# Kernel tuning notes

Measured on AMD Instinct MI355X. Metric: run time of the kernel, lower is better.

The kernel has to match this reference:

```python
import jax, jax.numpy as jnp
import numpy as np

R_EARTH = 6371.0


def haversine(coords):
    # coords: (B, N, 2) lat/lon in degrees -> (B, N, N) distances in km
    lat = jnp.deg2rad(coords[..., 0])
    lon = jnp.deg2rad(coords[..., 1])
    lat1, lon1 = lat[:, :, None], lon[:, :, None]   # (B,N,1)
    lat2, lon2 = lat[:, None, :], lon[:, None, :]   # (B,1,N)
    dlat, dlon = lat2 - lat1, lon2 - lon1
    a = jnp.sin(dlat / 2) ** 2 + jnp.cos(lat1) * jnp.cos(lat2) * jnp.sin(dlon / 2) ** 2
    a = jnp.clip(a, 0.0, 1.0)
    c = 2.0 * jnp.arctan2(jnp.sqrt(a), jnp.sqrt(1.0 - a))
    return R_EARTH * c


def setup_inputs() -> dict:
    key = jax.random.key(0)
    ks = jax.random.split(key, 16)
    B, N, T, D, H = 4, 256, 128, 512, 8
    hd = D // H
    s = 1.0 / np.sqrt(D)
    inp = {
        'x': jax.random.normal(ks[0], (B, N, T, D), dtype=jnp.float32),
        'coords': jax.random.uniform(ks[1], (B, N, 2), dtype=jnp.float32) * 90.0,
        'station_mask': jax.random.randint(ks[2], (B, N), 0, 2, dtype=jnp.int32),
        'Wq': jax.random.normal(ks[3], (D, D), dtype=jnp.float32) * s,
        'bq': jnp.zeros((D,), dtype=jnp.float32),
        'Wk': jax.random.normal(ks[4], (D, D), dtype=jnp.float32) * s,
        'bk': jnp.zeros((D,), dtype=jnp.float32),
        'Wv': jax.random.normal(ks[5], (D, D), dtype=jnp.float32) * s,
        'bv': jnp.zeros((D,), dtype=jnp.float32),
        'Wo': jax.random.normal(ks[6], (D, D), dtype=jnp.float32) * s,
        'bo': jnp.zeros((D,), dtype=jnp.float32),
        'Wd1': jax.random.normal(ks[7], (hd, 1), dtype=jnp.float32),
        'bd1': jnp.zeros((hd,), dtype=jnp.float32),
        'Wd2': jax.random.normal(ks[8], (H, hd), dtype=jnp.float32) / np.sqrt(hd),
        'bd2': jnp.zeros((H,), dtype=jnp.float32),
    }
    return inp


def reference(x, coords, station_mask, Wq, bq, Wk, bk, Wv, bv, Wo, bo, Wd1, bd1, Wd2, bd2):
    B, N, T, D = x.shape
    H = Wd2.shape[0]
    hd = D // H
    scale = jnp.sqrt(jnp.asarray(hd, dtype=x.dtype))

    x_repr = x.mean(axis=2)  # (B,N,D) temporal pooling

    def proj(W, b):
        y = x_repr @ W.T + b                       # (B,N,D)
        return y.reshape(B, N, H, hd).transpose(0, 2, 1, 3)  # (B,H,N,hd)

    Q, K, V = proj(Wq, bq), proj(Wk, bk), proj(Wv, bv)
    scores = jnp.einsum('bhnd,bhmd->bhnm', Q, K) / scale  # (B,H,N,N)

    # haversine distance -> 2-layer MLP bias, (B,N,N,H) -> (B,H,N,N)
    dist = haversine(coords)[..., None]                    # (B,N,N,1)
    hmid = jax.nn.relu(dist @ Wd1.T + bd1)                 # (B,N,N,hd)
    bias = (hmid @ Wd2.T + bd2).transpose(0, 3, 1, 2)      # (B,H,N,N)
    scores = scores + bias

    # mask invalid key stations
    scores = jnp.where(station_mask[:, None, None, :] == 0, -jnp.inf, scores)
    w = jax.nn.softmax(scores, axis=-1)

    out = jnp.einsum('bhnm,bhmd->bhnd', w, V)
    out = out.transpose(0, 2, 1, 3).reshape(B, N, D)
    out = out @ Wo.T + bo
    return jnp.broadcast_to(out[:, :, None, :], (B, N, T, D))
```

## Files before the change

kernel.cpp:

```cpp
#include <hip/hip_runtime.h>
#include <math.h>

#define Bc 4
#define Nc 256
#define Tc 128
#define Dc 512
#define Hc 8
#define HDc 64

__device__ __forceinline__ float4 f4add(float4 a, float4 b) {
    return make_float4(a.x + b.x, a.y + b.y, a.z + b.z, a.w + b.w);
}

#define SWZ(row, k4) (((row) << 4) | ((k4) ^ (((row) >> 2) & 15)))

__global__ __launch_bounds__(256) void mean_kernel(const float* __restrict__ x,
                                                   float* __restrict__ xr) {
    const int bn = blockIdx.x;
    const int col = threadIdx.x & 127;
    const int half = threadIdx.x >> 7;
    const float4* xp = (const float4*)x + (size_t)bn * (Tc * Dc / 4)
                       + (size_t)(half * 64) * (Dc / 4) + col;
    float4 a0 = make_float4(0.f, 0.f, 0.f, 0.f), a1 = a0, a2 = a0, a3 = a0;
    for (int t = 0; t < 64; t += 4) {
        a0 = f4add(a0, xp[(size_t)(t + 0) * (Dc / 4)]);
        a1 = f4add(a1, xp[(size_t)(t + 1) * (Dc / 4)]);
        a2 = f4add(a2, xp[(size_t)(t + 2) * (Dc / 4)]);
        a3 = f4add(a3, xp[(size_t)(t + 3) * (Dc / 4)]);
    }
    __shared__ float4 red[256];
    red[threadIdx.x] = f4add(f4add(a0, a1), f4add(a2, a3));
    __syncthreads();
    if (threadIdx.x < 128) {
        float4 s = f4add(red[threadIdx.x], red[threadIdx.x + 128]);
        const float r = 1.0f / Tc;
        ((float4*)xr)[(size_t)bn * (Dc / 4) + threadIdx.x] =
            make_float4(s.x * r, s.y * r, s.z * r, s.w * r);
    }
}

__device__ __forceinline__ void gemm_core(const float* __restrict__ A,
                                          const float* __restrict__ W,
                                          int i0, int j0, float acc[4][4]) {
    __shared__ float4 As4[1024];
    __shared__ float4 Ws4[1024];
    const int tid = threadIdx.x;
    const int ty = tid >> 4, tx = tid & 15;
    for (int kb = 0; kb < 8; ++kb) {
        const int k0 = kb * 64;
#pragma unroll
        for (int p = 0; p < 4; ++p) {
            const int idx = p * 256 + tid;
            const int row = idx >> 4, k4 = idx & 15;
            As4[SWZ(row, k4)] = *(const float4*)&A[(size_t)(i0 + row) * Dc + k0 + k4 * 4];
            Ws4[SWZ(row, k4)] = *(const float4*)&W[(size_t)(j0 + row) * Dc + k0 + k4 * 4];
        }
        __syncthreads();
#pragma unroll
        for (int kk4 = 0; kk4 < 16; ++kk4) {
            float4 a[4], w[4];
#pragma unroll
            for (int q = 0; q < 4; ++q) a[q] = As4[SWZ(ty * 4 + q, kk4)];
#pragma unroll
            for (int c = 0; c < 4; ++c) w[c] = Ws4[SWZ(tx * 4 + c, kk4)];
#pragma unroll
            for (int q = 0; q < 4; ++q)
#pragma unroll
                for (int c = 0; c < 4; ++c) {
                    acc[q][c] += a[q].x * w[c].x;
                    acc[q][c] += a[q].y * w[c].y;
                    acc[q][c] += a[q].z * w[c].z;
                    acc[q][c] += a[q].w * w[c].w;
                }
        }
        __syncthreads();
    }
}

__global__ __launch_bounds__(256) void qkv_kernel(
    const float* __restrict__ xr, const float* __restrict__ Wq, const float* __restrict__ bq,
    const float* __restrict__ Wk, const float* __restrict__ bk,
    const float* __restrict__ Wv, const float* __restrict__ bv,
    float* __restrict__ Yq, float* __restrict__ Kt, float* __restrict__ Yv) {
    const int it = blockIdx.x;
    const int mat = blockIdx.y >> 3;
    const int jt = blockIdx.y & 7;
    const float* W = (mat == 0) ? Wq : (mat == 1) ? Wk : Wv;
    const float* bias = (mat == 0) ? bq : (mat == 1) ? bk : bv;
    const int i0 = it * 64, j0 = jt * 64;
    float acc[4][4] = {{0.f}};
    gemm_core(xr, W, i0, j0, acc);
    const int ty = threadIdx.x >> 4, tx = threadIdx.x & 15;
    if (mat == 1) {
        const int b = i0 >> 8;
        const int n0 = (i0 & 255) + ty * 4;
#pragma unroll
        for (int c = 0; c < 4; ++c) {
            const int j = j0 + tx * 4 + c;
            const float bj = bias[j];
            float4 v = make_float4(acc[0][c] + bj, acc[1][c] + bj,
                                   acc[2][c] + bj, acc[3][c] + bj);
            *(float4*)&Kt[(((size_t)b * Hc + jt) * HDc + (tx * 4 + c)) * Nc + n0] = v;
        }
    } else {
        float* Y = (mat == 0) ? Yq : Yv;
#pragma unroll
        for (int r = 0; r < 4; ++r) {
            const int i = i0 + ty * 4 + r;
            const int j = j0 + tx * 4;
            float4 o = make_float4(acc[r][0] + bias[j + 0], acc[r][1] + bias[j + 1],
                                   acc[r][2] + bias[j + 2], acc[r][3] + bias[j + 3]);
            *(float4*)&Y[(size_t)i * Dc + j] = o;
        }
    }
}

__global__ __launch_bounds__(256) void oproj_kernel(const float* __restrict__ attn,
                                                    const float* __restrict__ Wo,
                                                    const float* __restrict__ bo,
                                                    float* __restrict__ Y) {
    const int i0 = blockIdx.x * 64, j0 = blockIdx.y * 64;
    float acc[4][4] = {{0.f}};
    gemm_core(attn, Wo, i0, j0, acc);
    const int ty = threadIdx.x >> 4, tx = threadIdx.x & 15;
#pragma unroll
    for (int r = 0; r < 4; ++r) {
        const int i = i0 + ty * 4 + r;
        const int j = j0 + tx * 4;
        float4 o = make_float4(acc[r][0] + bo[j + 0], acc[r][1] + bo[j + 1],
                               acc[r][2] + bo[j + 2], acc[r][3] + bo[j + 3]);
        *(float4*)&Y[(size_t)i * Dc + j] = o;
    }
}

__global__ __launch_bounds__(256) void bias_kernel(
    const float* __restrict__ coords, const int* __restrict__ mask,
    const float* __restrict__ Wd1, const float* __restrict__ bd1,
    const float* __restrict__ Wd2, const float* __restrict__ bd2,
    float* __restrict__ biasb) {
    const int b = blockIdx.x >> 8;
    const int n = blockIdx.x & 255;
    const int m = threadIdx.x;
    __shared__ float swd1[64], sbd1[64], swd2[512], sbd2[8];
    if (threadIdx.x < 64) {
        swd1[threadIdx.x] = Wd1[threadIdx.x];
        sbd1[threadIdx.x] = bd1[threadIdx.x];
    }
    if (threadIdx.x < 8) sbd2[threadIdx.x] = bd2[threadIdx.x];
    swd2[threadIdx.x] = Wd2[threadIdx.x];
    swd2[threadIdx.x + 256] = Wd2[threadIdx.x + 256];
    __syncthreads();

    const float DEG = 0.017453292519943295f;
    float lat1 = coords[((size_t)b * Nc + n) * 2 + 0] * DEG;
    float lon1 = coords[((size_t)b * Nc + n) * 2 + 1] * DEG;
    float lat2 = coords[((size_t)b * Nc + m) * 2 + 0] * DEG;
    float lon2 = coords[((size_t)b * Nc + m) * 2 + 1] * DEG;
    float sdlat = sinf((lat2 - lat1) * 0.5f);
    float sdlon = sinf((lon2 - lon1) * 0.5f);
    float a = sdlat * sdlat + cosf(lat1) * cosf(lat2) * sdlon * sdlon;
    a = fminf(fmaxf(a, 0.0f), 1.0f);
    float c = 2.0f * atan2f(sqrtf(a), sqrtf(1.0f - a));
    float dist = 6371.0f * c;

    float acc[8];
#pragma unroll
    for (int h = 0; h < 8; ++h) acc[h] = sbd2[h];
#pragma unroll 8
    for (int k = 0; k < 64; ++k) {
        float hm = fmaxf(dist * swd1[k] + sbd1[k], 0.0f);
#pragma unroll
        for (int h = 0; h < 8; ++h) acc[h] += hm * swd2[h * 64 + k];
    }
    const bool masked = (mask[(size_t)b * Nc + m] == 0);
#pragma unroll
    for (int h = 0; h < 8; ++h) {
        biasb[(((size_t)(b * Hc + h) * Nc + n) * Nc) + m] = masked ? -1e30f : acc[h];
    }
}

__global__ __launch_bounds__(256) void attn_kernel(
    const float* __restrict__ Yq, const float* __restrict__ Kt,
    const float* __restrict__ Yv, const float* __restrict__ biasb,
    float* __restrict__ attnO) {
    const int bh = blockIdx.x >> 6;
    const int ng = blockIdx.x & 63;
    const int b = bh >> 3, h = bh & 7;
    const int wave = threadIdx.x >> 6;
    const int lane = threadIdx.x & 63;
    const int n = ng * 4 + wave;

    __shared__ float sq[4][64];
    __shared__ float sw[4][256];

    sq[wave][lane] = Yq[((size_t)(b * Nc + n)) * Dc + h * HDc + lane] * 0.125f;
    __syncthreads();

    const float4* ktp = (const float4*)(Kt + (size_t)bh * HDc * Nc);
    float4 acc = make_float4(0.f, 0.f, 0.f, 0.f);
#pragma unroll 16
    for (int k = 0; k < 64; ++k) {
        const float qk = sq[wave][k];
        const float4 kv = ktp[k * 64 + lane];
        acc.x += qk * kv.x; acc.y += qk * kv.y;
        acc.z += qk * kv.z; acc.w += qk * kv.w;
    }
    const float4 bi = ((const float4*)(biasb + ((size_t)bh * Nc + n) * Nc))[lane];
    float4 s = make_float4(acc.x + bi.x, acc.y + bi.y, acc.z + bi.z, acc.w + bi.w);
    float mx = fmaxf(fmaxf(s.x, s.y), fmaxf(s.z, s.w));
#pragma unroll
    for (int off = 32; off > 0; off >>= 1) mx = fmaxf(mx, __shfl_xor(mx, off, 64));

    float4 e = make_float4(expf(s.x - mx), expf(s.y - mx), expf(s.z - mx), expf(s.w - mx));
    ((float4*)sw[wave])[lane] = e;
    float sum = e.x + e.y + e.z + e.w;
#pragma unroll
    for (int off = 32; off > 0; off >>= 1) sum += __shfl_xor(sum, off, 64);
    const float inv = 1.0f / sum;
    __syncthreads();

    float o = 0.f;
    const float* vb = Yv + (size_t)b * Nc * Dc + h * HDc + lane;
    const float4* sw4 = (const float4*)sw[wave];
#pragma unroll 8
    for (int mq = 0; mq < 64; ++mq) {
        float4 w4 = sw4[mq];
        const int m = mq * 4;
        o += w4.x * vb[(size_t)(m + 0) * Dc];
        o += w4.y * vb[(size_t)(m + 1) * Dc];
        o += w4.z * vb[(size_t)(m + 2) * Dc];
        o += w4.w * vb[(size_t)(m + 3) * Dc];
    }
    attnO[((size_t)(b * Nc + n)) * Dc + h * HDc + lane] = o * inv;
}

__global__ __launch_bounds__(256) void bcast_kernel(const float* __restrict__ y,
                                                    float* __restrict__ out) {
    const int bn = blockIdx.x >> 1;
    const int half = blockIdx.x & 1;
    __shared__ float4 row[128];
    if (threadIdx.x < 128) row[threadIdx.x] = ((const float4*)y)[(size_t)bn * 128 + threadIdx.x];
    __syncthreads();
    float4* op = (float4*)out + (size_t)bn * (Tc * Dc / 4) + (size_t)half * 8192;
#pragma unroll 4
    for (int it = 0; it < 32; ++it) {
        const int idx = it * 256 + threadIdx.x;
        op[idx] = row[idx & 127];
    }
}

extern "C" void kernel_launch(void* const* d_in, const int* in_sizes, int n_in,
                              void* d_out, int out_size, void* d_ws, size_t ws_size,
                              hipStream_t stream) {
    const float* x      = (const float*)d_in[0];
    const float* coords = (const float*)d_in[1];
    const int*   smask  = (const int*)d_in[2];
    const float* Wq = (const float*)d_in[3];  const float* bq = (const float*)d_in[4];
    const float* Wk = (const float*)d_in[5];  const float* bk = (const float*)d_in[6];
    const float* Wv = (const float*)d_in[7];  const float* bv = (const float*)d_in[8];
    const float* Wo = (const float*)d_in[9];  const float* bo = (const float*)d_in[10];
    const float* Wd1 = (const float*)d_in[11]; const float* bd1 = (const float*)d_in[12];
    const float* Wd2 = (const float*)d_in[13]; const float* bd2 = (const float*)d_in[14];
    float* out = (float*)d_out;

    float* ws    = (float*)d_ws;
    const size_t BND = (size_t)Bc * Nc * Dc;
    float* xr    = ws;
    float* Yq    = xr + BND;
    float* Kt    = Yq + BND;
    float* Yv    = Kt + BND;
    float* biasb = Yv + BND;
    float* attn  = biasb + (size_t)Bc * Hc * Nc * Nc;
    float* yout  = attn + BND;

    mean_kernel<<<Bc * Nc, 256, 0, stream>>>(x, xr);
    qkv_kernel<<<dim3(16, 24), 256, 0, stream>>>(xr, Wq, bq, Wk, bk, Wv, bv, Yq, Kt, Yv);
    bias_kernel<<<Bc * Nc, 256, 0, stream>>>(coords, smask, Wd1, bd1, Wd2, bd2, biasb);
    attn_kernel<<<Bc * Hc * (Nc / 4), 256, 0, stream>>>(Yq, Kt, Yv, biasb, attn);
    oproj_kernel<<<dim3(16, 8), 256, 0, stream>>>(attn, Wo, bo, yout);
    bcast_kernel<<<2 * Bc * Nc, 256, 0, stream>>>(yout, out);
}
```

Before: 602.4 us.

## Fuse distance bias into attention and broadcast into output projection, prefetch GEMM tiles

The haversine distance and MLP bias are now computed inside the attention kernel, so the B*H*N*N bias buffer is no longer written and read back. The output projection writes its result broadcast across T directly with nontemporal stores, which removes the separate broadcast kernel and its intermediate buffer. Several smaller changes come with this: register prefetch of the next k-tile in the shared GEMM core, a wider unroll with nontemporal loads in the mean kernel, and a float4 V-accumulation with cross-lane reduction in attention. The cost is that the bias MLP is recomputed per head and the projection GEMM is computed twice, once for each half of the z grid.

```diff
diff --git a/kernel.cpp b/kernel.cpp
--- a/kernel.cpp
+++ b/kernel.cpp
@@ -8,9 +8,7 @@
 #define Hc 8
 #define HDc 64
 
-__device__ __forceinline__ float4 f4add(float4 a, float4 b) {
-    return make_float4(a.x + b.x, a.y + b.y, a.z + b.z, a.w + b.w);
-}
+typedef float f4v __attribute__((ext_vector_type(4)));
 
 #define SWZ(row, k4) (((row) << 4) | ((k4) ^ (((row) >> 2) & 15)))
 
@@ -19,23 +17,23 @@
     const int bn = blockIdx.x;
     const int col = threadIdx.x & 127;
     const int half = threadIdx.x >> 7;
-    const float4* xp = (const float4*)x + (size_t)bn * (Tc * Dc / 4)
-                       + (size_t)(half * 64) * (Dc / 4) + col;
-    float4 a0 = make_float4(0.f, 0.f, 0.f, 0.f), a1 = a0, a2 = a0, a3 = a0;
-    for (int t = 0; t < 64; t += 4) {
-        a0 = f4add(a0, xp[(size_t)(t + 0) * (Dc / 4)]);
-        a1 = f4add(a1, xp[(size_t)(t + 1) * (Dc / 4)]);
-        a2 = f4add(a2, xp[(size_t)(t + 2) * (Dc / 4)]);
-        a3 = f4add(a3, xp[(size_t)(t + 3) * (Dc / 4)]);
-    }
-    __shared__ float4 red[256];
-    red[threadIdx.x] = f4add(f4add(a0, a1), f4add(a2, a3));
+    const f4v* xp = (const f4v*)x + (size_t)bn * (Tc * Dc / 4)
+                    + (size_t)(half * 64) * (Dc / 4) + col;
+    f4v a[8];
+#pragma unroll
+    for (int u = 0; u < 8; ++u) a[u] = (f4v)(0.f);
+    for (int t = 0; t < 64; t += 8) {
+#pragma unroll
+        for (int u = 0; u < 8; ++u)
+            a[u] += __builtin_nontemporal_load(xp + (size_t)(t + u) * (Dc / 4));
+    }
+    f4v s = ((a[0] + a[1]) + (a[2] + a[3])) + ((a[4] + a[5]) + (a[6] + a[7]));
+    __shared__ f4v red[256];
+    red[threadIdx.x] = s;
     __syncthreads();
     if (threadIdx.x < 128) {
-        float4 s = f4add(red[threadIdx.x], red[threadIdx.x + 128]);
-        const float r = 1.0f / Tc;
-        ((float4*)xr)[(size_t)bn * (Dc / 4) + threadIdx.x] =
-            make_float4(s.x * r, s.y * r, s.z * r, s.w * r);
+        f4v r = (red[threadIdx.x] + red[threadIdx.x + 128]) * (1.0f / Tc);
+        ((f4v*)xr)[(size_t)bn * (Dc / 4) + threadIdx.x] = r;
     }
 }
 
@@ -46,16 +44,27 @@
     __shared__ float4 Ws4[1024];
     const int tid = threadIdx.x;
     const int ty = tid >> 4, tx = tid & 15;
+    float4 pa[4], pw[4];
+#pragma unroll
+    for (int p = 0; p < 4; ++p) {
+        pa[p] = *(const float4*)&A[(size_t)(i0 + p * 16 + ty) * Dc + tx * 4];
+        pw[p] = *(const float4*)&W[(size_t)(j0 + p * 16 + ty) * Dc + tx * 4];
+    }
     for (int kb = 0; kb < 8; ++kb) {
-        const int k0 = kb * 64;
 #pragma unroll
         for (int p = 0; p < 4; ++p) {
-            const int idx = p * 256 + tid;
-            const int row = idx >> 4, k4 = idx & 15;
-            As4[SWZ(row, k4)] = *(const float4*)&A[(size_t)(i0 + row) * Dc + k0 + k4 * 4];
-            Ws4[SWZ(row, k4)] = *(const float4*)&W[(size_t)(j0 + row) * Dc + k0 + k4 * 4];
+            As4[SWZ(p * 16 + ty, tx)] = pa[p];
+            Ws4[SWZ(p * 16 + ty, tx)] = pw[p];
         }
         __syncthreads();
+        if (kb < 7) {
+            const int k0 = (kb + 1) * 64;
+#pragma unroll
+            for (int p = 0; p < 4; ++p) {
+                pa[p] = *(const float4*)&A[(size_t)(i0 + p * 16 + ty) * Dc + k0 + tx * 4];
+                pw[p] = *(const float4*)&W[(size_t)(j0 + p * 16 + ty) * Dc + k0 + tx * 4];
+            }
+        }
 #pragma unroll
         for (int kk4 = 0; kk4 < 16; ++kk4) {
             float4 a[4], w[4];
@@ -115,84 +124,37 @@
     }
 }
 
-__global__ __launch_bounds__(256) void oproj_kernel(const float* __restrict__ attn,
-                                                    const float* __restrict__ Wo,
-                                                    const float* __restrict__ bo,
-                                                    float* __restrict__ Y) {
-    const int i0 = blockIdx.x * 64, j0 = blockIdx.y * 64;
-    float acc[4][4] = {{0.f}};
-    gemm_core(attn, Wo, i0, j0, acc);
-    const int ty = threadIdx.x >> 4, tx = threadIdx.x & 15;
-#pragma unroll
-    for (int r = 0; r < 4; ++r) {
-        const int i = i0 + ty * 4 + r;
-        const int j = j0 + tx * 4;
-        float4 o = make_float4(acc[r][0] + bo[j + 0], acc[r][1] + bo[j + 1],
-                               acc[r][2] + bo[j + 2], acc[r][3] + bo[j + 3]);
-        *(float4*)&Y[(size_t)i * Dc + j] = o;
-    }
-}
-
-__global__ __launch_bounds__(256) void bias_kernel(
-    const float* __restrict__ coords, const int* __restrict__ mask,
-    const float* __restrict__ Wd1, const float* __restrict__ bd1,
-    const float* __restrict__ Wd2, const float* __restrict__ bd2,
-    float* __restrict__ biasb) {
-    const int b = blockIdx.x >> 8;
-    const int n = blockIdx.x & 255;
-    const int m = threadIdx.x;
-    __shared__ float swd1[64], sbd1[64], swd2[512], sbd2[8];
-    if (threadIdx.x < 64) {
-        swd1[threadIdx.x] = Wd1[threadIdx.x];
-        sbd1[threadIdx.x] = bd1[threadIdx.x];
-    }
-    if (threadIdx.x < 8) sbd2[threadIdx.x] = bd2[threadIdx.x];
-    swd2[threadIdx.x] = Wd2[threadIdx.x];
-    swd2[threadIdx.x + 256] = Wd2[threadIdx.x + 256];
-    __syncthreads();
-
-    const float DEG = 0.017453292519943295f;
-    float lat1 = coords[((size_t)b * Nc + n) * 2 + 0] * DEG;
-    float lon1 = coords[((size_t)b * Nc + n) * 2 + 1] * DEG;
-    float lat2 = coords[((size_t)b * Nc + m) * 2 + 0] * DEG;
-    float lon2 = coords[((size_t)b * Nc + m) * 2 + 1] * DEG;
-    float sdlat = sinf((lat2 - lat1) * 0.5f);
-    float sdlon = sinf((lon2 - lon1) * 0.5f);
-    float a = sdlat * sdlat + cosf(lat1) * cosf(lat2) * sdlon * sdlon;
-    a = fminf(fmaxf(a, 0.0f), 1.0f);
-    float c = 2.0f * atan2f(sqrtf(a), sqrtf(1.0f - a));
-    float dist = 6371.0f * c;
-
-    float acc[8];
-#pragma unroll
-    for (int h = 0; h < 8; ++h) acc[h] = sbd2[h];
-#pragma unroll 8
-    for (int k = 0; k < 64; ++k) {
-        float hm = fmaxf(dist * swd1[k] + sbd1[k], 0.0f);
-#pragma unroll
-        for (int h = 0; h < 8; ++h) acc[h] += hm * swd2[h * 64 + k];
-    }
-    const bool masked = (mask[(size_t)b * Nc + m] == 0);
-#pragma unroll
-    for (int h = 0; h < 8; ++h) {
-        biasb[(((size_t)(b * Hc + h) * Nc + n) * Nc) + m] = masked ? -1e30f : acc[h];
-    }
-}
-
 __global__ __launch_bounds__(256) void attn_kernel(
     const float* __restrict__ Yq, const float* __restrict__ Kt,
-    const float* __restrict__ Yv, const float* __restrict__ biasb,
-    float* __restrict__ attnO) {
+    const float* __restrict__ Yv, const float* __restrict__ coords,
+    const int* __restrict__ mask, const float* __restrict__ Wd1,
+    const float* __restrict__ bd1, const float* __restrict__ Wd2,
+    const float* __restrict__ bd2, float* __restrict__ attnO) {
     const int bh = blockIdx.x >> 6;
     const int ng = blockIdx.x & 63;
     const int b = bh >> 3, h = bh & 7;
-    const int wave = threadIdx.x >> 6;
-    const int lane = threadIdx.x & 63;
+    const int tid = threadIdx.x;
+    const int wave = tid >> 6, lane = tid & 63;
     const int n = ng * 4 + wave;
 
     __shared__ float sq[4][64];
     __shared__ float sw[4][256];
-
+    __shared__ float slat[256], slon[256], scl[256];
+    __shared__ float swd1[64], sbd1[64], swd2[64];
+    __shared__ int smk[256];
+
+    {
+        const float DEG = 0.017453292519943295f;
+        float la = coords[((size_t)b * Nc + tid) * 2 + 0] * DEG;
+        float lo = coords[((size_t)b * Nc + tid) * 2 + 1] * DEG;
+        slat[tid] = la; slon[tid] = lo; scl[tid] = cosf(la);
+        smk[tid] = mask[(size_t)b * Nc + tid];
+        if (tid < 64) {
+            swd1[tid] = Wd1[tid];
+            sbd1[tid] = bd1[tid];
+            swd2[tid] = Wd2[h * 64 + tid];
+        }
+    }
     sq[wave][lane] = Yq[((size_t)(b * Nc + n)) * Dc + h * HDc + lane] * 0.125f;
     __syncthreads();
 
@@ -205,47 +167,98 @@
         acc.x += qk * kv.x; acc.y += qk * kv.y;
         acc.z += qk * kv.z; acc.w += qk * kv.w;
     }
-    const float4 bi = ((const float4*)(biasb + ((size_t)bh * Nc + n) * Nc))[lane];
-    float4 s = make_float4(acc.x + bi.x, acc.y + bi.y, acc.z + bi.z, acc.w + bi.w);
-    float mx = fmaxf(fmaxf(s.x, s.y), fmaxf(s.z, s.w));
+
+    const float lat1 = slat[n], lon1 = slon[n], cl1 = scl[n];
+    float dist[4];
+#pragma unroll
+    for (int j = 0; j < 4; ++j) {
+        const int m = lane * 4 + j;
+        float sdlat = sinf((slat[m] - lat1) * 0.5f);
+        float sdlon = sinf((slon[m] - lon1) * 0.5f);
+        float a = sdlat * sdlat + cl1 * scl[m] * sdlon * sdlon;
+        a = fminf(fmaxf(a, 0.f), 1.f);
+        dist[j] = 12742.0f * atan2f(sqrtf(a), sqrtf(1.0f - a));
+    }
+    const float b2 = bd2[h];
+    float bias[4] = {b2, b2, b2, b2};
+#pragma unroll 4
+    for (int k = 0; k < 64; ++k) {
+        const float w1 = swd1[k], c1 = sbd1[k], w2 = swd2[k];
+#pragma unroll
+        for (int j = 0; j < 4; ++j)
+            bias[j] += fmaxf(dist[j] * w1 + c1, 0.f) * w2;
+    }
+    float s[4] = {acc.x + bias[0], acc.y + bias[1], acc.z + bias[2], acc.w + bias[3]};
+#pragma unroll
+    for (int j = 0; j < 4; ++j)
+        if (smk[lane * 4 + j] == 0) s[j] = -1e30f;
+
+    float mx = fmaxf(fmaxf(s[0], s[1]), fmaxf(s[2], s[3]));
 #pragma unroll
     for (int off = 32; off > 0; off >>= 1) mx = fmaxf(mx, __shfl_xor(mx, off, 64));
-
-    float4 e = make_float4(expf(s.x - mx), expf(s.y - mx), expf(s.z - mx), expf(s.w - mx));
-    ((float4*)sw[wave])[lane] = e;
-    float sum = e.x + e.y + e.z + e.w;
+    float e0 = expf(s[0] - mx), e1 = expf(s[1] - mx);
+    float e2 = expf(s[2] - mx), e3 = expf(s[3] - mx);
+    ((float4*)sw[wave])[lane] = make_float4(e0, e1, e2, e3);
+    float sum = e0 + e1 + e2 + e3;
 #pragma unroll
     for (int off = 32; off > 0; off >>= 1) sum += __shfl_xor(sum, off, 64);
     const float inv = 1.0f / sum;
     __syncthreads();
 
-    float o = 0.f;
-    const float* vb = Yv + (size_t)b * Nc * Dc + h * HDc + lane;
-    const float4* sw4 = (const float4*)sw[wave];
+    const int mo = lane >> 4, d4 = lane & 15;
+    const float* vbase = Yv + (size_t)b * Nc * Dc + h * HDc + d4 * 4;
+    const float* wv = sw[wave];
+    float4 o = make_float4(0.f, 0.f, 0.f, 0.f);
 #pragma unroll 8
     for (int mq = 0; mq < 64; ++mq) {
-        float4 w4 = sw4[mq];
-        const int m = mq * 4;
-        o += w4.x * vb[(size_t)(m + 0) * Dc];
-        o += w4.y * vb[(size_t)(m + 1) * Dc];
-        o += w4.z * vb[(size_t)(m + 2) * Dc];
-        o += w4.w * vb[(size_t)(m + 3) * Dc];
-    }
-    attnO[((size_t)(b * Nc + n)) * Dc + h * HDc + lane] = o * inv;
-}
-
-__global__ __launch_bounds__(256) void bcast_kernel(const float* __restrict__ y,
-                                                    float* __restrict__ out) {
-    const int bn = blockIdx.x >> 1;
-    const int half = blockIdx.x & 1;
-    __shared__ float4 row[128];
-    if (threadIdx.x < 128) row[threadIdx.x] = ((const float4*)y)[(size_t)bn * 128 + threadIdx.x];
-    __syncthreads();
-    float4* op = (float4*)out + (size_t)bn * (Tc * Dc / 4) + (size_t)half * 8192;
-#pragma unroll 4
-    for (int it = 0; it < 32; ++it) {
-        const int idx = it * 256 + threadIdx.x;
-        op[idx] = row[idx & 127];
+        const int m = mq * 4 + mo;
+        const float wm = wv[m];
+        const float4 v = *(const float4*)&vbase[(size_t)m * Dc];
+        o.x += wm * v.x; o.y += wm * v.y; o.z += wm * v.z; o.w += wm * v.w;
+    }
+#pragma unroll
+    for (int off = 16; off <= 32; off <<= 1) {
+        o.x += __shfl_xor(o.x, off, 64);
+        o.y += __shfl_xor(o.y, off, 64);
+        o.z += __shfl_xor(o.z, off, 64);
+        o.w += __shfl_xor(o.w, off, 64);
+    }
+    if (mo == 0) {
+        float4 r = make_float4(o.x * inv, o.y * inv, o.z * inv, o.w * inv);
+        *(float4*)&attnO[((size_t)(b * Nc + n)) * Dc + h * HDc + d4 * 4] = r;
+    }
+}
+
+__global__ __launch_bounds__(256) void oproj_bcast_kernel(
+    const float* __restrict__ attnI, const float* __restrict__ Wo,
+    const float* __restrict__ bo, float* __restrict__ out) {
+    const int i0 = blockIdx.x * 64, j0 = blockIdx.y * 64;
+    const int z = blockIdx.z;
+    float acc[4][4] = {{0.f}};
+    gemm_core(attnI, Wo, i0, j0, acc);
+
+    __shared__ f4v tile[1024];
+    const int ty = threadIdx.x >> 4, tx = threadIdx.x & 15;
+#pragma unroll
+    for (int q = 0; q < 4; ++q) {
+        const int j = j0 + tx * 4;
+        f4v v;
+        v.x = acc[q][0] + bo[j + 0]; v.y = acc[q][1] + bo[j + 1];
+        v.z = acc[q][2] + bo[j + 2]; v.w = acc[q][3] + bo[j + 3];
+        tile[(ty * 4 + q) * 16 + tx] = v;
+    }
+    __syncthreads();
+
+    const int d4 = threadIdx.x & 15;
+    const int sub = threadIdx.x >> 4;
+    for (int r = 0; r < 64; ++r) {
+        const f4v val = tile[r * 16 + d4];
+        float* rowbase = out + (size_t)(i0 + r) * Tc * Dc + j0;
+#pragma unroll
+        for (int tt = 0; tt < 4; ++tt) {
+            const int t = z * 64 + tt * 16 + sub;
+            __builtin_nontemporal_store(val, (f4v*)(rowbase + (size_t)t * Dc) + d4);
+        }
     }
 }
 
@@ -269,14 +282,11 @@
     float* Yq    = xr + BND;
     float* Kt    = Yq + BND;
     float* Yv    = Kt + BND;
-    float* biasb = Yv + BND;
-    float* attn  = biasb + (size_t)Bc * Hc * Nc * Nc;
-    float* yout  = attn + BND;
+    float* attn  = Yv + BND;
 
     mean_kernel<<<Bc * Nc, 256, 0, stream>>>(x, xr);
     qkv_kernel<<<dim3(16, 24), 256, 0, stream>>>(xr, Wq, bq, Wk, bk, Wv, bv, Yq, Kt, Yv);
-    bias_kernel<<<Bc * Nc, 256, 0, stream>>>(coords, smask, Wd1, bd1, Wd2, bd2, biasb);
-    attn_kernel<<<Bc * Hc * (Nc / 4), 256, 0, stream>>>(Yq, Kt, Yv, biasb, attn);
-    oproj_kernel<<<dim3(16, 8), 256, 0, stream>>>(attn, Wo, bo, yout);
-    bcast_kernel<<<2 * Bc * Nc, 256, 0, stream>>>(yout, out);
-}
+    attn_kernel<<<Bc * Hc * (Nc / 4), 256, 0, stream>>>(Yq, Kt, Yv, coords, smask,
+                                                        Wd1, bd1, Wd2, bd2, attn);
+    oproj_bcast_kernel<<<dim3(16, 8, 2), 256, 0, stream>>>(attn, Wo, bo, out);
+}
```

Measured after the change: 594.5 us. About the same (-1.3%).
